# Kernel optimization log

Measured on AMD Instinct MI355X. Metric: run time of the kernel, lower is better.

Reference implementation:

```python
import jax, jax.numpy as jnp
import numpy as np
import math

LENGTH = 2048
N_LEVEL = int(math.log2(LENGTH))   # 11 butterfly levels
BATCH = 4096
CROSS_T = 1.0      # crossing_transmission_factor (ideal)
CROSS_PHI = 0.0    # crossing_phase_shift (ideal)


def _bitrev(n):
    perm = np.arange(n).reshape(n, 1)
    for _ in range(int(math.log2(n))):
        h = perm.shape[0] // 2
        perm = np.hstack((perm[:h], perm[h:]))
    return perm.squeeze(0)


def _forward_indices(length):
    # ButterflyPermutation.gen_permutation_indices (forward direction)
    nlev = int(math.log2(length)) - 1
    init = np.arange(length)
    idxs = []
    for level in range(nlev):
        bs = 2 ** (level + 2)
        idx = init.reshape(-1, length // bs, 2, bs // 2).transpose(0, 1, 3, 2).reshape(-1)
        idxs.append(idx)
    return idxs


def _crossings(idxs, length):
    # cascaded waveguide-crossing transfer function per level: [length, 2] complex
    out = []
    for idx in idxs:
        n = np.abs(idx - np.arange(length)).astype(np.float32)
        mag = CROSS_T ** n
        phi = n * CROSS_PHI
        out.append(np.stack([mag * np.cos(phi), mag * np.sin(phi)], -1).astype(np.float32))
    return out


BITREV = _bitrev(LENGTH)
FWD_IDX = _forward_indices(LENGTH)
CROSSINGS = [jnp.asarray(c) for c in _crossings(FWD_IDX, LENGTH)]


def complex_mult(a, b):
    ar, ai = a[..., 0], a[..., 1]
    br, bi = b[..., 0], b[..., 1]
    return jnp.stack([ar * br - ai * bi, ar * bi + ai * br], axis=-1)


def setup_inputs() -> dict:
    key = jax.random.key(0)
    kx, kp = jax.random.split(key)
    x = jax.random.normal(kx, (BATCH, LENGTH, 2), dtype=jnp.float32)
    phases = jax.random.normal(kp, (N_LEVEL + 1, LENGTH // 2, 2), dtype=jnp.float32)
    return {"x": x, "phases": phases}


def reference(x, phases):
    # mode='full' coupler transfer function (build_coupler_transfer_function_2)
    ph = phases[:N_LEVEL]                      # [n_level, L/2, 2]
    c1, c2 = jnp.cos(ph[..., 0]), jnp.cos(ph[..., 1])
    s1, s2 = jnp.sin(ph[..., 0]), jnp.sin(ph[..., 1])
    w_real = jnp.stack([c1, -s2, -s1, c2], -1).reshape(N_LEVEL, LENGTH // 2, 2, 2)
    w_imag = jnp.stack([s1, c2, c1, s2], -1).reshape(N_LEVEL, LENGTH // 2, 2, 2)

    out = x[:, BITREV, :]                      # bit-reversal permutation
    for level in range(N_LEVEL):
        v = out.reshape(BATCH, LENGTH // 2, 2, 2)   # [b, pair, j, complex]
        vr, vi = v[..., 0], v[..., 1]
        wr, wi = w_real[level], w_imag[level]
        # complex 2x2 matvec per pair
        r = jnp.einsum('pij,bpj->bpi', wr, vr) - jnp.einsum('pij,bpj->bpi', wi, vi)
        i = jnp.einsum('pij,bpj->bpi', wr, vi) + jnp.einsum('pij,bpj->bpi', wi, vr)
        out = jnp.stack([r, i], -1).reshape(BATCH, LENGTH, 2)
        if level < N_LEVEL - 1:
            # butterfly permutation + crossing transfer (identity when ideal)
            out = complex_mult(CROSSINGS[level][None], out[:, FWD_IDX[level], :])

    # last-level phase shifter: one phase per waveguide
    lp = phases[-1].reshape(LENGTH)
    ps = jnp.stack([jnp.cos(lp), jnp.sin(lp)], -1)  # [L, 2]
    return complex_mult(ps[None], out)
```

## Files before the change

kernel.cpp:

```cpp
#include <hip/hip_runtime.h>


__device__ __forceinline__ unsigned revw(unsigned x, int w) {
    return w ? (__brev(x) >> (32 - w)) : 0u;
}

__global__ void twiddle_kernel(const float* __restrict__ phases, float4* __restrict__ tw) {
    int id = blockIdx.x * 256 + threadIdx.x;
    float t1, t2;
    if (id < 1024) {
        unsigned p = revw((unsigned)id, 10);
        t1 = phases[p * 2 + 0]; t2 = phases[p * 2 + 1];
    } else if (id < 10240) {
        int j = id - 1024;
        int sg = j / 3072;
        int rem = j % 3072;
        int m = rem >> 8;
        int u = rem & 255;
        int L = 3 * sg + 1;
        int lvl_off = m >> 2;
        int pj = m & 3;
        int c;
        if (lvl_off == 0) c = pj;
        else if (lvl_off == 1) c = (pj & 1) | ((pj >> 1) << 2);
        else c = pj << 1;
        unsigned h = 1u << (8 - L);
        unsigned s = (((unsigned)u >> (8 - L)) << (11 - L)) | ((unsigned)u & (h - 1));
        unsigned slot = s + (unsigned)c * h;
        int level = L + lvl_off;
        int shift = 10 - level;
        unsigned p = (revw(slot & ((1u << shift) - 1u), shift) << level) | (slot >> (shift + 1));
        const float* ph = phases + (level * 1024 + p) * 2;
        t1 = ph[0]; t2 = ph[1];
    } else if (id < 11264) {
        unsigned v = id - 10240;
        const float* ph = phases + (10 * 1024 + v) * 2;
        t1 = ph[0]; t2 = ph[1];
    } else if (id < 12288) {
        int q = id - 11264;
        const float* lp = phases + 11 * 2048 + q * 2;
        t1 = lp[0]; t2 = lp[1];
    } else {
        return;
    }
    tw[id] = make_float4(cosf(t1), sinf(t1), cosf(t2), sinf(t2));
}

__device__ __forceinline__ void bf(float2 v0, float2 v1, float4 w, float2& o0, float2& o1) {
    float ar = fmaf(w.x, v0.x, -w.y * v0.y);
    float ai = fmaf(w.x, v0.y,  w.y * v0.x);
    float br = fmaf(w.z, v1.x, -w.w * v1.y);
    float bi = fmaf(w.z, v1.y,  w.w * v1.x);
    o0 = make_float2(ar - bi, ai + br);
    o1 = make_float2(br - ai, bi + ar);
}

__device__ __forceinline__ unsigned swz(unsigned U) { return U ^ ((U >> 3) & 7u); }
__device__ __forceinline__ float2 ld2(const float4* lds, unsigned e) {
    return ((const float2*)lds)[swz(e >> 1) * 2 + (e & 1)];
}
__device__ __forceinline__ void st2(float4* lds, unsigned e, float2 v) {
    ((float2*)lds)[swz(e >> 1) * 2 + (e & 1)] = v;
}

__device__ __forceinline__ void radix8_compute(float2 e[8], const float4 W[12]) {
    float2 a[8], b[8];
    bf(e[0], e[4], W[0], a[0], a[4]);
    bf(e[1], e[5], W[1], a[1], a[5]);
    bf(e[2], e[6], W[2], a[2], a[6]);
    bf(e[3], e[7], W[3], a[3], a[7]);
    bf(a[0], a[2], W[4], b[0], b[2]);
    bf(a[1], a[3], W[5], b[1], b[3]);
    bf(a[4], a[6], W[6], b[4], b[6]);
    bf(a[5], a[7], W[7], b[5], b[7]);
    bf(b[0], b[1], W[8],  e[0], e[1]);
    bf(b[2], b[3], W[9],  e[2], e[3]);
    bf(b[4], b[5], W[10], e[4], e[5]);
    bf(b[6], b[7], W[11], e[6], e[7]);
}

template <int L>
__device__ __forceinline__ void radix8_stage(float4* l0, float4* l1,
                                             const float4* __restrict__ tw, int t) {
    constexpr unsigned h = 1u << (8 - L);
    constexpr int base = 1024 + ((L - 1) / 3) * 3072;
    const unsigned u = (unsigned)t;
    const unsigned s = ((u >> (8 - L)) << (11 - L)) | (u & (h - 1));
    float4 W[12];
#pragma unroll
    for (int m = 0; m < 12; ++m) W[m] = tw[base + m * 256 + u];
    float2 e0[8], e1[8];
#pragma unroll
    for (int j = 0; j < 8; ++j) e0[j] = ld2(l0, s + j * h);
#pragma unroll
    for (int j = 0; j < 8; ++j) e1[j] = ld2(l1, s + j * h);
    radix8_compute(e0, W);
    radix8_compute(e1, W);
#pragma unroll
    for (int j = 0; j < 8; ++j) st2(l0, s + j * h, e0[j]);
#pragma unroll
    for (int j = 0; j < 8; ++j) st2(l1, s + j * h, e1[j]);
}

__global__ __launch_bounds__(256) void bfly_kernel(const float4* __restrict__ x,
                                                   const float4* __restrict__ tw,
                                                   float4* __restrict__ out) {
    __shared__ float4 lds[2048];
    const int t = threadIdx.x;
    const int rowbase = blockIdx.x * 2048;
    float4* l0 = lds;
    float4* l1 = lds + 1024;

#pragma unroll
    for (int k = 0; k < 2; ++k) {
        unsigned v = (unsigned)t + 256u * k;
        float4 w0 = tw[2 * v], w1 = tw[2 * v + 1];
#pragma unroll
        for (int r = 0; r < 2; ++r) {
            const float4* xr = x + rowbase + r * 1024;
            float4 q0 = xr[v];
            float4 q1 = xr[v + 512];
            float2 o0a, o1a, o0b, o1b;
            bf(make_float2(q0.x, q0.y), make_float2(q1.x, q1.y), w0, o0a, o1a);
            bf(make_float2(q0.z, q0.w), make_float2(q1.z, q1.w), w1, o0b, o1b);
            float4* lr = r ? l1 : l0;
            lr[swz(v)]       = make_float4(o0a.x, o0a.y, o0b.x, o0b.y);
            lr[swz(v + 512)] = make_float4(o1a.x, o1a.y, o1b.x, o1b.y);
        }
    }
    __syncthreads();

    radix8_stage<1>(l0, l1, tw, t); __syncthreads();
    radix8_stage<4>(l0, l1, tw, t); __syncthreads();
    radix8_stage<7>(l0, l1, tw, t); __syncthreads();

#pragma unroll
    for (int g = 0; g < 4; ++g) {
        unsigned v = (unsigned)t + 256u * g;
        float4 wf = tw[10240 + v];
        float4 wp = tw[11264 + v];
#pragma unroll
        for (int r = 0; r < 2; ++r) {
            float4 q = (r ? l1 : l0)[swz(v)];
            float2 o0, o1;
            bf(make_float2(q.x, q.y), make_float2(q.z, q.w), wf, o0, o1);
            out[rowbase + r * 1024 + v] = make_float4(
                fmaf(wp.x, o0.x, -wp.y * o0.y), fmaf(wp.x, o0.y, wp.y * o0.x),
                fmaf(wp.z, o1.x, -wp.w * o1.y), fmaf(wp.z, o1.y, wp.w * o1.x));
        }
    }
}

extern "C" void kernel_launch(void* const* d_in, const int* in_sizes, int n_in,
                              void* d_out, int out_size, void* d_ws, size_t ws_size,
                              hipStream_t stream) {
    const float* x = (const float*)d_in[0];
    const float* phases = (const float*)d_in[1];
    float4* tw = (float4*)d_ws;

    twiddle_kernel<<<48, 256, 0, stream>>>(phases, tw);
    bfly_kernel<<<2048, 256, 0, stream>>>((const float4*)x, tw, (float4*)d_out);
}
```

Before: 40.12 us.

## Regroup butterfly levels into 2+3+3+3 register stages with new LDS swizzle

Restructures the in-block butterfly schedule. The first two levels are now done in registers straight from global loads, then come two radix-8 LDS stages, and the last three levels plus the phase shift are done in registers before contiguous stores. The twiddle table is reorganised to match this new level grouping. The LDS swizzle now XORs two bit groups, and launch bounds request 5 blocks per CU. Twiddles are loaded per level to reduce register pressure, at the cost of more complex index mapping in the twiddle kernel.

```diff
diff --git a/kernel.cpp b/kernel.cpp
--- a/kernel.cpp
+++ b/kernel.cpp
@@ -4,44 +4,60 @@
 __device__ __forceinline__ unsigned revw(unsigned x, int w) {
     return w ? (__brev(x) >> (32 - w)) : 0u;
 }
+__device__ __forceinline__ unsigned pmap(unsigned slot, int level) {
+    int shift = 10 - level;
+    return (revw(slot & ((1u << shift) - 1u), shift) << level) | (slot >> (shift + 1));
+}
 
 __global__ void twiddle_kernel(const float* __restrict__ phases, float4* __restrict__ tw) {
     int id = blockIdx.x * 256 + threadIdx.x;
+    if (id >= 12288) return;
     float t1, t2;
-    if (id < 1024) {
-        unsigned p = revw((unsigned)id, 10);
-        t1 = phases[p * 2 + 0]; t2 = phases[p * 2 + 1];
+    if (id < 2048) {
+        int t = id & 255, r = id >> 8;
+        int b = r & 1, pj = (r >> 1) & 1, lvl = r >> 2;
+        unsigned unit = (unsigned)t + ((lvl == 0) ? 256u : 512u) * (unsigned)pj;
+        unsigned slot = 2u * unit + (unsigned)b;
+        unsigned p = pmap(slot, lvl);
+        t1 = phases[(lvl * 1024 + p) * 2 + 0];
+        t2 = phases[(lvl * 1024 + p) * 2 + 1];
+    } else if (id < 8192) {
+        int j2 = id - 2048;
+        int sg = j2 / 3072, rem = j2 % 3072;
+        int m = rem >> 8, t = rem & 255;
+        int L = 2 + 3 * sg;
+        int lg = sg ? 3 : 6;
+        unsigned H = 1u << lg;
+        unsigned s = (((unsigned)t >> lg) << (lg + 3)) | ((unsigned)t & (H - 1));
+        int lo = m >> 2, pj = m & 3;
+        int j = (lo == 0) ? pj : ((lo == 1) ? ((pj & 1) | ((pj >> 1) << 2)) : (pj << 1));
+        unsigned slot = s + (unsigned)j * H;
+        int level = L + lo;
+        unsigned p = pmap(slot, level);
+        t1 = phases[(level * 1024 + p) * 2 + 0];
+        t2 = phases[(level * 1024 + p) * 2 + 1];
+    } else if (id < 9216) {
+        int i = id - 8192;
+        unsigned slot = 8u * (unsigned)(i >> 2) + (unsigned)(i & 3);
+        unsigned p = pmap(slot, 8);
+        t1 = phases[(8 * 1024 + p) * 2 + 0];
+        t2 = phases[(8 * 1024 + p) * 2 + 1];
     } else if (id < 10240) {
-        int j = id - 1024;
-        int sg = j / 3072;
-        int rem = j % 3072;
-        int m = rem >> 8;
-        int u = rem & 255;
-        int L = 3 * sg + 1;
-        int lvl_off = m >> 2;
-        int pj = m & 3;
-        int c;
-        if (lvl_off == 0) c = pj;
-        else if (lvl_off == 1) c = (pj & 1) | ((pj >> 1) << 2);
-        else c = pj << 1;
-        unsigned h = 1u << (8 - L);
-        unsigned s = (((unsigned)u >> (8 - L)) << (11 - L)) | ((unsigned)u & (h - 1));
-        unsigned slot = s + (unsigned)c * h;
-        int level = L + lvl_off;
-        int shift = 10 - level;
-        unsigned p = (revw(slot & ((1u << shift) - 1u), shift) << level) | (slot >> (shift + 1));
-        const float* ph = phases + (level * 1024 + p) * 2;
-        t1 = ph[0]; t2 = ph[1];
+        int i = id - 9216;
+        int m = i & 3;
+        unsigned slot = 8u * (unsigned)(i >> 2) + (unsigned)(((m >> 1) << 2) | (m & 1));
+        unsigned p = pmap(slot, 9);
+        t1 = phases[(9 * 1024 + p) * 2 + 0];
+        t2 = phases[(9 * 1024 + p) * 2 + 1];
     } else if (id < 11264) {
-        unsigned v = id - 10240;
-        const float* ph = phases + (10 * 1024 + v) * 2;
-        t1 = ph[0]; t2 = ph[1];
-    } else if (id < 12288) {
+        unsigned w = (unsigned)(id - 10240);
+        unsigned p = pmap(2u * w, 10);
+        t1 = phases[(10 * 1024 + p) * 2 + 0];
+        t2 = phases[(10 * 1024 + p) * 2 + 1];
+    } else {
         int q = id - 11264;
-        const float* lp = phases + 11 * 2048 + q * 2;
-        t1 = lp[0]; t2 = lp[1];
-    } else {
-        return;
+        t1 = phases[11 * 2048 + q * 2 + 0];
+        t2 = phases[11 * 2048 + q * 2 + 1];
     }
     tw[id] = make_float4(cosf(t1), sinf(t1), cosf(t2), sinf(t2));
 }
@@ -55,98 +71,138 @@
     o1 = make_float2(br - ai, bi + ar);
 }
 
-__device__ __forceinline__ unsigned swz(unsigned U) { return U ^ ((U >> 3) & 7u); }
-__device__ __forceinline__ float2 ld2(const float4* lds, unsigned e) {
-    return ((const float2*)lds)[swz(e >> 1) * 2 + (e & 1)];
-}
-__device__ __forceinline__ void st2(float4* lds, unsigned e, float2 v) {
-    ((float2*)lds)[swz(e >> 1) * 2 + (e & 1)] = v;
-}
-
-__device__ __forceinline__ void radix8_compute(float2 e[8], const float4 W[12]) {
-    float2 a[8], b[8];
-    bf(e[0], e[4], W[0], a[0], a[4]);
-    bf(e[1], e[5], W[1], a[1], a[5]);
-    bf(e[2], e[6], W[2], a[2], a[6]);
-    bf(e[3], e[7], W[3], a[3], a[7]);
-    bf(a[0], a[2], W[4], b[0], b[2]);
-    bf(a[1], a[3], W[5], b[1], b[3]);
-    bf(a[4], a[6], W[6], b[4], b[6]);
-    bf(a[5], a[7], W[7], b[5], b[7]);
-    bf(b[0], b[1], W[8],  e[0], e[1]);
-    bf(b[2], b[3], W[9],  e[2], e[3]);
-    bf(b[4], b[5], W[10], e[4], e[5]);
-    bf(b[6], b[7], W[11], e[6], e[7]);
-}
-
-template <int L>
-__device__ __forceinline__ void radix8_stage(float4* l0, float4* l1,
-                                             const float4* __restrict__ tw, int t) {
-    constexpr unsigned h = 1u << (8 - L);
-    constexpr int base = 1024 + ((L - 1) / 3) * 3072;
-    const unsigned u = (unsigned)t;
-    const unsigned s = ((u >> (8 - L)) << (11 - L)) | (u & (h - 1));
-    float4 W[12];
-#pragma unroll
-    for (int m = 0; m < 12; ++m) W[m] = tw[base + m * 256 + u];
+__device__ __forceinline__ unsigned swz(unsigned U) {
+    return U ^ (((U >> 3) ^ (U >> 6)) & 7u);
+}
+__device__ __forceinline__ float2 ld2(const float4* l, unsigned c) {
+    return ((const float2*)l)[swz(c >> 1) * 2 + (c & 1)];
+}
+__device__ __forceinline__ void st2(float4* l, unsigned c, float2 v) {
+    ((float2*)l)[swz(c >> 1) * 2 + (c & 1)] = v;
+}
+
+__device__ __forceinline__ void lvlA(float2 e[8], const float4 w[4]) {
+    bf(e[0], e[4], w[0], e[0], e[4]);
+    bf(e[1], e[5], w[1], e[1], e[5]);
+    bf(e[2], e[6], w[2], e[2], e[6]);
+    bf(e[3], e[7], w[3], e[3], e[7]);
+}
+__device__ __forceinline__ void lvlB(float2 e[8], const float4 w[4]) {
+    bf(e[0], e[2], w[0], e[0], e[2]);
+    bf(e[1], e[3], w[1], e[1], e[3]);
+    bf(e[4], e[6], w[2], e[4], e[6]);
+    bf(e[5], e[7], w[3], e[5], e[7]);
+}
+__device__ __forceinline__ void lvlC(float2 e[8], const float4 w[4]) {
+    bf(e[0], e[1], w[0], e[0], e[1]);
+    bf(e[2], e[3], w[1], e[2], e[3]);
+    bf(e[4], e[5], w[2], e[4], e[5]);
+    bf(e[6], e[7], w[3], e[6], e[7]);
+}
+
+template <int SG>
+__device__ __forceinline__ void sstage(float4* l0, float4* l1,
+                                       const float4* __restrict__ tw, unsigned t) {
+    constexpr unsigned LG = SG ? 3u : 6u;
+    constexpr unsigned H = 1u << LG;
+    constexpr int base = SG ? 5120 : 2048;
+    const unsigned s = ((t >> LG) << (LG + 3)) | (t & (H - 1));
     float2 e0[8], e1[8];
 #pragma unroll
-    for (int j = 0; j < 8; ++j) e0[j] = ld2(l0, s + j * h);
-#pragma unroll
-    for (int j = 0; j < 8; ++j) e1[j] = ld2(l1, s + j * h);
-    radix8_compute(e0, W);
-    radix8_compute(e1, W);
-#pragma unroll
-    for (int j = 0; j < 8; ++j) st2(l0, s + j * h, e0[j]);
-#pragma unroll
-    for (int j = 0; j < 8; ++j) st2(l1, s + j * h, e1[j]);
-}
-
-__global__ __launch_bounds__(256) void bfly_kernel(const float4* __restrict__ x,
-                                                   const float4* __restrict__ tw,
-                                                   float4* __restrict__ out) {
+    for (int j = 0; j < 8; ++j) e0[j] = ld2(l0, s + H * j);
+#pragma unroll
+    for (int j = 0; j < 8; ++j) e1[j] = ld2(l1, s + H * j);
+    float4 w[4];
+#pragma unroll
+    for (int k = 0; k < 4; ++k) w[k] = tw[base + k * 256 + t];
+    lvlA(e0, w); lvlA(e1, w);
+#pragma unroll
+    for (int k = 0; k < 4; ++k) w[k] = tw[base + (4 + k) * 256 + t];
+    lvlB(e0, w); lvlB(e1, w);
+#pragma unroll
+    for (int k = 0; k < 4; ++k) w[k] = tw[base + (8 + k) * 256 + t];
+    lvlC(e0, w); lvlC(e1, w);
+#pragma unroll
+    for (int j = 0; j < 8; ++j) st2(l0, s + H * j, e0[j]);
+#pragma unroll
+    for (int j = 0; j < 8; ++j) st2(l1, s + H * j, e1[j]);
+}
+
+__global__ __launch_bounds__(256, 5) void bfly_kernel(const float4* __restrict__ x,
+                                                      const float4* __restrict__ tw,
+                                                      float4* __restrict__ out) {
     __shared__ float4 lds[2048];
-    const int t = threadIdx.x;
+    const unsigned t = threadIdx.x;
     const int rowbase = blockIdx.x * 2048;
     float4* l0 = lds;
     float4* l1 = lds + 1024;
 
-#pragma unroll
-    for (int k = 0; k < 2; ++k) {
-        unsigned v = (unsigned)t + 256u * k;
-        float4 w0 = tw[2 * v], w1 = tw[2 * v + 1];
-#pragma unroll
-        for (int r = 0; r < 2; ++r) {
-            const float4* xr = x + rowbase + r * 1024;
-            float4 q0 = xr[v];
-            float4 q1 = xr[v + 512];
-            float2 o0a, o1a, o0b, o1b;
-            bf(make_float2(q0.x, q0.y), make_float2(q1.x, q1.y), w0, o0a, o1a);
-            bf(make_float2(q0.z, q0.w), make_float2(q1.z, q1.w), w1, o0b, o1b);
-            float4* lr = r ? l1 : l0;
-            lr[swz(v)]       = make_float4(o0a.x, o0a.y, o0b.x, o0b.y);
-            lr[swz(v + 512)] = make_float4(o1a.x, o1a.y, o1b.x, o1b.y);
+    {
+        const float4* x0 = x + rowbase;
+        const float4* x1 = x + rowbase + 1024;
+        float2 z0[8], z1[8];
+#pragma unroll
+        for (int k = 0; k < 4; ++k) {
+            float4 u = x0[t + 256u * k];
+            z0[2 * k] = make_float2(u.x, u.y); z0[2 * k + 1] = make_float2(u.z, u.w);
+        }
+#pragma unroll
+        for (int k = 0; k < 4; ++k) {
+            float4 u = x1[t + 256u * k];
+            z1[2 * k] = make_float2(u.x, u.y); z1[2 * k + 1] = make_float2(u.z, u.w);
+        }
+        float4 w[4];
+#pragma unroll
+        for (int k = 0; k < 4; ++k) w[k] = tw[k * 256 + t];
+        lvlA(z0, w); lvlA(z1, w);
+#pragma unroll
+        for (int k = 0; k < 4; ++k) w[k] = tw[(4 + k) * 256 + t];
+        lvlB(z0, w); lvlB(z1, w);
+#pragma unroll
+        for (int k = 0; k < 4; ++k) {
+            l0[swz(t + 256u * k)] = make_float4(z0[2 * k].x, z0[2 * k].y, z0[2 * k + 1].x, z0[2 * k + 1].y);
+            l1[swz(t + 256u * k)] = make_float4(z1[2 * k].x, z1[2 * k].y, z1[2 * k + 1].x, z1[2 * k + 1].y);
         }
     }
     __syncthreads();
 
-    radix8_stage<1>(l0, l1, tw, t); __syncthreads();
-    radix8_stage<4>(l0, l1, tw, t); __syncthreads();
-    radix8_stage<7>(l0, l1, tw, t); __syncthreads();
-
-#pragma unroll
-    for (int g = 0; g < 4; ++g) {
-        unsigned v = (unsigned)t + 256u * g;
-        float4 wf = tw[10240 + v];
-        float4 wp = tw[11264 + v];
-#pragma unroll
-        for (int r = 0; r < 2; ++r) {
-            float4 q = (r ? l1 : l0)[swz(v)];
-            float2 o0, o1;
-            bf(make_float2(q.x, q.y), make_float2(q.z, q.w), wf, o0, o1);
-            out[rowbase + r * 1024 + v] = make_float4(
-                fmaf(wp.x, o0.x, -wp.y * o0.y), fmaf(wp.x, o0.y, wp.y * o0.x),
-                fmaf(wp.z, o1.x, -wp.w * o1.y), fmaf(wp.z, o1.y, wp.w * o1.x));
+    sstage<0>(l0, l1, tw, t);
+    __syncthreads();
+    sstage<1>(l0, l1, tw, t);
+    __syncthreads();
+
+    {
+        float2 z0[8], z1[8];
+#pragma unroll
+        for (int k = 0; k < 4; ++k) {
+            float4 u = l0[swz(4u * t + k)];
+            z0[2 * k] = make_float2(u.x, u.y); z0[2 * k + 1] = make_float2(u.z, u.w);
+            u = l1[swz(4u * t + k)];
+            z1[2 * k] = make_float2(u.x, u.y); z1[2 * k + 1] = make_float2(u.z, u.w);
+        }
+        float4 w[4];
+#pragma unroll
+        for (int i = 0; i < 4; ++i) w[i] = tw[8192 + 4u * t + i];
+        lvlA(z0, w); lvlA(z1, w);
+#pragma unroll
+        for (int i = 0; i < 4; ++i) w[i] = tw[9216 + 4u * t + i];
+        lvlB(z0, w); lvlB(z1, w);
+#pragma unroll
+        for (int i = 0; i < 4; ++i) w[i] = tw[10240 + 4u * t + i];
+        lvlC(z0, w); lvlC(z1, w);
+#pragma unroll
+        for (int k = 0; k < 4; ++k) {
+            float4 p = tw[11264 + 4u * t + k];
+            out[rowbase + 4u * t + k] = make_float4(
+                fmaf(p.x, z0[2 * k].x, -p.y * z0[2 * k].y),
+                fmaf(p.x, z0[2 * k].y,  p.y * z0[2 * k].x),
+                fmaf(p.z, z0[2 * k + 1].x, -p.w * z0[2 * k + 1].y),
+                fmaf(p.z, z0[2 * k + 1].y,  p.w * z0[2 * k + 1].x));
+            out[rowbase + 1024 + 4u * t + k] = make_float4(
+                fmaf(p.x, z1[2 * k].x, -p.y * z1[2 * k].y),
+                fmaf(p.x, z1[2 * k].y,  p.y * z1[2 * k].x),
+                fmaf(p.z, z1[2 * k + 1].x, -p.w * z1[2 * k + 1].y),
+                fmaf(p.z, z1[2 * k + 1].y,  p.w * z1[2 * k + 1].x));
         }
     }
 }
```

Measured after the change: 54.61 us. 1.36x slower.
